# Optimization experiments

Measured on AMD Instinct MI355X. Metric: run time of the kernel, lower is better.

## Reference

```python
import jax, jax.numpy as jnp
import numpy as np

B, N, D = 2, 2048, 1024   # batch, seq, input_dim
H, DK, DV = 8, 128, 1024  # heads, qk_dim, v_dim (v_dim == input_dim for residual)


def setup_inputs() -> dict:
    key = jax.random.key(0)
    kx, kq, kk, kv = jax.random.split(key, 4)
    scale = 0.02
    x = jax.random.normal(kx, (B, N, D), dtype=jnp.float32)
    # torch nn.Linear weights are [out_features, in_features]; stacked over heads.
    Wq = jax.random.normal(kq, (H, DK, D), dtype=jnp.float32) * scale
    Wk = jax.random.normal(kk, (H, DK, D), dtype=jnp.float32) * scale
    Wv = jax.random.normal(kv, (H, DV, D), dtype=jnp.float32) * scale
    return {"x": x, "Wq": Wq, "Wk": Wk, "Wv": Wv}


def reference(x, Wq, Wk, Wv):
    # x: [B, N, D]; Wq/Wk: [H, DK, D]; Wv: [H, DV, D]
    n = x.shape[-2]
    Q = jnp.einsum('bnd,hed->bhne', x, Wq)  # [B,H,N,DK]
    K = jnp.einsum('bnd,hed->bhne', x, Wk)  # [B,H,N,DK]
    V = jnp.einsum('bnd,hvd->bhnv', x, Wv)  # [B,H,N,DV]
    scores = jnp.einsum('bhne,bhme->bhnm', Q, K)  # [B,H,N,N]
    # causal mask: masked entries set to mask_value=0.0, then relu, then /N
    causal = jnp.tril(jnp.ones((n, n), dtype=bool))
    sim = jnp.where(causal, jax.nn.relu(scores), jnp.float32(0.0)) / jnp.float32(n)
    # sum of per-head outputs added to residual
    head_out = jnp.einsum('bhnm,bhmv->bnv', sim, V)  # [B,N,DV]
    return x + head_out
```

## Files before the change

### kernel.cpp

```cpp
#include <hip/hip_runtime.h>

typedef __attribute__((ext_vector_type(8))) short bf16x8;
typedef __attribute__((ext_vector_type(4))) float floatx4;

__device__ __forceinline__ unsigned short f2bf(float f) {
  unsigned int u = __builtin_bit_cast(unsigned int, f);
  unsigned int r = (u + 0x7fffu + ((u >> 16) & 1u)) >> 16;
  return (unsigned short)r;
}

__device__ __forceinline__ unsigned int pack2(float a, float b) {
  return (unsigned int)f2bf(a) | ((unsigned int)f2bf(b) << 16);
}

__device__ __forceinline__ void gload16(const void* g, void* l) {
  __builtin_amdgcn_global_load_lds(
      (__attribute__((address_space(1))) void*)g,
      (__attribute__((address_space(3))) void*)l, 16, 0, 0);
}

__device__ __forceinline__ void barrier_v0_lgkm() {
  asm volatile("s_waitcnt vmcnt(0) lgkmcnt(0)" ::: "memory");
  __builtin_amdgcn_s_barrier();
  __builtin_amdgcn_sched_barrier(0);
}

__global__ __launch_bounds__(256) void convert_all(
    const float4* __restrict__ x4,
    const float4* __restrict__ wq4, const float4* __restrict__ wk4,
    const float4* __restrict__ wv4,
    uint2* __restrict__ xb4, uint2* __restrict__ wqkb4, uint2* __restrict__ wvb4,
    float4* __restrict__ out4)
{
  const int NX = 2 * 2048 * 1024 / 4;
  const int NQK = 8 * 256 * 1024 / 4;
  const int NV = 8 * 1024 * 1024 / 4;
  const int total = NX + NQK + NV;
  const float inv_n = 1.0f / 2048.0f;
  for (int i = blockIdx.x * 256 + threadIdx.x; i < total; i += gridDim.x * 256) {
    float4 f; uint2* dst;
    if (i < NX) {
      f = x4[i]; dst = &xb4[i];
      out4[i] = f;
    } else if (i < NX + NQK) {
      int j = i - NX;
      int c = j & 255;
      int row = j >> 8;
      int h = row >> 8, r = row & 255;
      f = (r < 128) ? wq4[(h * 128 + r) * 256 + c] : wk4[(h * 128 + r - 128) * 256 + c];
      dst = &wqkb4[j];
    } else {
      int j = i - NX - NQK;
      f = wv4[j];
      f.x *= inv_n; f.y *= inv_n; f.z *= inv_n; f.w *= inv_n;
      dst = &wvb4[j];
    }
    uint2 p; p.x = pack2(f.x, f.y); p.y = pack2(f.z, f.w);
    *dst = p;
  }
}

__global__ __launch_bounds__(256) void init_out(const float4* __restrict__ x,
                                                float4* __restrict__ out, int n4) {
  for (int i = blockIdx.x * 256 + threadIdx.x; i < n4; i += gridDim.x * 256)
    out[i] = x[i];
}

__device__ __forceinline__ void gemm_body(
    const unsigned short* __restrict__ Ag,
    const unsigned short* __restrict__ Bg,
    unsigned short* __restrict__ C, long ld,
    unsigned short* LA, unsigned short* LB, int t)
{
  const int l = t & 63, w = t >> 6;
  const int wr = w >> 1, wc = w & 1;
  const int l16 = l & 15, lq = l >> 4;
  floatx4 acc[4][4] = {};
  for (int k0 = 0; k0 < 1024; k0 += 64) {
    __syncthreads();
    for (int i = 0; i < 4; i++) {
      int cbase = i * 256 + (t & 192);
      int chunk = cbase + (t & 63);
      int row = chunk >> 3, c8 = chunk & 7;
      gload16(Ag + (long)row * 1024 + k0 + c8 * 8, &LA[cbase * 8]);
      gload16(Bg + (long)row * 1024 + k0 + c8 * 8, &LB[cbase * 8]);
    }
    __syncthreads();
    for (int kk = 0; kk < 2; kk++) {
      bf16x8 af[4], bfr[4];
      for (int m = 0; m < 4; m++)
        af[m]  = *reinterpret_cast<const bf16x8*>(&LA[(wr * 64 + m * 16 + l16) * 64 + kk * 32 + lq * 8]);
      for (int n = 0; n < 4; n++)
        bfr[n] = *reinterpret_cast<const bf16x8*>(&LB[(wc * 64 + n * 16 + l16) * 64 + kk * 32 + lq * 8]);
      for (int m = 0; m < 4; m++)
        for (int n = 0; n < 4; n++)
          acc[m][n] = __builtin_amdgcn_mfma_f32_16x16x32_bf16(af[m], bfr[n], acc[m][n], 0, 0, 0);
    }
  }
  for (int m = 0; m < 4; m++)
    for (int n = 0; n < 4; n++)
      for (int j = 0; j < 4; j++) {
        int row = wr * 64 + m * 16 + lq * 4 + j;
        int col = wc * 64 + n * 16 + l16;
        C[(long)row * ld + col] = f2bf(acc[m][n][j]);
      }
}

__global__ __launch_bounds__(256) void gemm_all(
    const unsigned short* __restrict__ xb,
    const unsigned short* __restrict__ Wqkb,
    const unsigned short* __restrict__ Wvb,
    unsigned short* __restrict__ Qb, unsigned short* __restrict__ Kb,
    unsigned short* __restrict__ Vtb)
{
  __shared__ __align__(16) unsigned short LA[128 * 64];
  __shared__ __align__(16) unsigned short LB[128 * 64];
  const int bid = blockIdx.x;
  const int t = threadIdx.x;
  if (bid < 512) {
    int bx = bid & 15, qy = (bid >> 4) & 1, z = bid >> 5;
    int b = z >> 3, h = z & 7;
    const unsigned short* Ag = xb + (long)b * 2048 * 1024 + (long)bx * 128 * 1024;
    const unsigned short* Bg = Wqkb + (long)h * 256 * 1024 + (long)qy * 128 * 1024;
    unsigned short* C = (qy ? Kb : Qb) + (long)z * 2048 * 128 + (long)bx * 128 * 128;
    gemm_body(Ag, Bg, C, 128, LA, LB, t);
  } else {
    int v = bid - 512;
    int by = v & 15, bx = (v >> 4) & 7, z = v >> 7;
    int b = z >> 3, h = z & 7;
    const unsigned short* Ag = Wvb + (long)h * 1024 * 1024 + (long)bx * 128 * 1024;
    const unsigned short* Bg = xb + (long)b * 2048 * 1024 + (long)by * 128 * 1024;
    unsigned short* C = Vtb + (long)z * 1024 * 2048 + (long)bx * 128 * 2048 + by * 128;
    gemm_body(Ag, Bg, C, 2048, LA, LB, t);
  }
}

__global__ __launch_bounds__(256) void gemm_bt(
    const float* __restrict__ Abase, long sAb, long sAh,
    const float* __restrict__ Bbase, long sBb, long sBh,
    unsigned short* __restrict__ Cbase, long sC,
    int M, int Nc, int K, int H, float cscale)
{
  int z = blockIdx.z;
  int b = z / H, h = z % H;
  const float* A  = Abase + (long)b * sAb + (long)h * sAh;
  const float* Bm = Bbase + (long)b * sBb + (long)h * sBh;
  unsigned short* C = Cbase + (long)z * sC;
  int tRow = blockIdx.x * 128;
  int tCol = blockIdx.y * 128;
  __shared__ __align__(16) unsigned short LA[128 * 72];
  __shared__ __align__(16) unsigned short LB[128 * 72];
  int t = threadIdx.x;
  int l = t & 63, w = t >> 6;
  int wr = w >> 1, wc = w & 1;
  int l16 = l & 15, lq = l >> 4;
  floatx4 acc[4][4] = {};
  for (int k0 = 0; k0 < K; k0 += 64) {
    __syncthreads();
    for (int i = 0; i < 8; i++) {
      int lin = i * 256 + t;
      int row = lin >> 4;
      int c4  = lin & 15;
      float4 va = *reinterpret_cast<const float4*>(A + (long)(tRow + row) * K + k0 + c4 * 4);
      uint2 pa; pa.x = pack2(va.x, va.y); pa.y = pack2(va.z, va.w);
      *reinterpret_cast<uint2*>(&LA[row * 72 + c4 * 4]) = pa;
      float4 vb = *reinterpret_cast<const float4*>(Bm + (long)(tCol + row) * K + k0 + c4 * 4);
      uint2 pb; pb.x = pack2(vb.x, vb.y); pb.y = pack2(vb.z, vb.w);
      *reinterpret_cast<uint2*>(&LB[row * 72 + c4 * 4]) = pb;
    }
    __syncthreads();
    for (int kk = 0; kk < 2; kk++) {
      bf16x8 af[4], bfr[4];
      for (int m = 0; m < 4; m++)
        af[m]  = *reinterpret_cast<const bf16x8*>(&LA[(wr * 64 + m * 16 + l16) * 72 + kk * 32 + lq * 8]);
      for (int n = 0; n < 4; n++)
        bfr[n] = *reinterpret_cast<const bf16x8*>(&LB[(wc * 64 + n * 16 + l16) * 72 + kk * 32 + lq * 8]);
      for (int m = 0; m < 4; m++)
        for (int n = 0; n < 4; n++)
          acc[m][n] = __builtin_amdgcn_mfma_f32_16x16x32_bf16(af[m], bfr[n], acc[m][n], 0, 0, 0);
    }
  }
  for (int m = 0; m < 4; m++)
    for (int n = 0; n < 4; n++)
      for (int j = 0; j < 4; j++) {
        int row = tRow + wr * 64 + m * 16 + lq * 4 + j;
        int col = tCol + wc * 64 + n * 16 + l16;
        C[(long)row * Nc + col] = f2bf(acc[m][n][j] * cscale);
      }
}

__global__ __launch_bounds__(256) void gemm_qk(
    const float* __restrict__ x,
    const float* __restrict__ Wq, const float* __restrict__ Wk,
    unsigned short* __restrict__ Qb, unsigned short* __restrict__ Kb)
{
  int z = blockIdx.z;
  int b = z >> 3, h = z & 7;
  const float* A  = x + (long)b * 2048 * 1024;
  const float* Bm = (blockIdx.y ? Wk : Wq) + (long)h * 128 * 1024;
  unsigned short* C = (blockIdx.y ? Kb : Qb) + (long)z * 2048 * 128;
  int tRow = blockIdx.x * 128;
  __shared__ __align__(16) unsigned short LA[128 * 72];
  __shared__ __align__(16) unsigned short LB[128 * 72];
  int t = threadIdx.x;
  int l = t & 63, w = t >> 6;
  int wr = w >> 1, wc = w & 1;
  int l16 = l & 15, lq = l >> 4;
  floatx4 acc[4][4] = {};
  const int K = 1024;
  for (int k0 = 0; k0 < K; k0 += 64) {
    __syncthreads();
    for (int i = 0; i < 8; i++) {
      int lin = i * 256 + t;
      int row = lin >> 4;
      int c4  = lin & 15;
      float4 va = *reinterpret_cast<const float4*>(A + (long)(tRow + row) * K + k0 + c4 * 4);
      uint2 pa; pa.x = pack2(va.x, va.y); pa.y = pack2(va.z, va.w);
      *reinterpret_cast<uint2*>(&LA[row * 72 + c4 * 4]) = pa;
      float4 vb = *reinterpret_cast<const float4*>(Bm + (long)row * K + k0 + c4 * 4);
      uint2 pb; pb.x = pack2(vb.x, vb.y); pb.y = pack2(vb.z, vb.w);
      *reinterpret_cast<uint2*>(&LB[row * 72 + c4 * 4]) = pb;
    }
    __syncthreads();
    for (int kk = 0; kk < 2; kk++) {
      bf16x8 af[4], bfr[4];
      for (int m = 0; m < 4; m++)
        af[m]  = *reinterpret_cast<const bf16x8*>(&LA[(wr * 64 + m * 16 + l16) * 72 + kk * 32 + lq * 8]);
      for (int n = 0; n < 4; n++)
        bfr[n] = *reinterpret_cast<const bf16x8*>(&LB[(wc * 64 + n * 16 + l16) * 72 + kk * 32 + lq * 8]);
      for (int m = 0; m < 4; m++)
        for (int n = 0; n < 4; n++)
          acc[m][n] = __builtin_amdgcn_mfma_f32_16x16x32_bf16(af[m], bfr[n], acc[m][n], 0, 0, 0);
    }
  }
  for (int m = 0; m < 4; m++)
    for (int n = 0; n < 4; n++)
      for (int j = 0; j < 4; j++) {
        int row = tRow + wr * 64 + m * 16 + lq * 4 + j;
        int col = wc * 64 + n * 16 + l16;
        C[(long)row * 128 + col] = f2bf(acc[m][n][j]);
      }
}

__global__ __launch_bounds__(256, 2) void attn_fused(
    const unsigned short* __restrict__ Qb,
    const unsigned short* __restrict__ Kb,
    const unsigned short* __restrict__ Vtb,
    float* __restrict__ out)
{
  const int bid = blockIdx.x;
  const int z = bid & 15;
  const int pair = (bid >> 4) & 15;
  const int vb = bid >> 8;
  const int b = z >> 3;
  const int t = threadIdx.x;
  const int l = t & 63, w = t >> 6;
  const int l16 = l & 15, lq = l >> 4;
  const int wm = w & 1, wn = w >> 1;
  const int swz = l16 & 7;

  __shared__ __align__(16) unsigned short LK[2][64 * 128];
  __shared__ __align__(16) unsigned short LV[256 * 64];
  __shared__ __align__(16) unsigned short LP[64 * 64];

  const unsigned short* Qz = Qb + (long)z * 2048 * 128;
  const unsigned short* Kh = Kb + (long)z * 2048 * 128;
  const unsigned short* Vh = Vtb + (long)z * 1024 * 2048 + (long)(vb * 256) * 2048;

  int ksrc[4], kdst[4];
#pragma unroll
  for (int i = 0; i < 4; i++) {
    int chunk = i * 256 + w * 64 + l;
    int r = chunk >> 4, c = chunk & 15;
    int cs = ((c & 7) ^ (r & 7)) | (c & 8);
    ksrc[i] = r * 128 + cs * 8;
    kdst[i] = (i * 256 + w * 64) * 8;
  }
  int vsrc[8], vdst[8];
#pragma unroll
  for (int i = 0; i < 8; i++) {
    int chunk = i * 256 + w * 64 + l;
    int r = chunk >> 3, c = chunk & 7;
    int cs = c ^ (r & 7);
    vsrc[i] = r * 2048 + cs * 8;
    vdst[i] = (i * 256 + w * 64) * 8;
  }

  int cur = 0;
  for (int hf = 0; hf < 2; hf++) {
    const int T = hf ? (31 - pair) : pair;
    const unsigned short* Qh = Qz + (long)T * 64 * 128;
    bf16x8 aQ[2][4];
#pragma unroll
    for (int sn = 0; sn < 2; sn++)
#pragma unroll
      for (int ke = 0; ke < 4; ke++)
        aQ[sn][ke] = *reinterpret_cast<const bf16x8*>(
            Qh + (long)(wn * 32 + sn * 16 + l16) * 128 + ke * 32 + lq * 8);
    floatx4 acc[4][4] = {};
#pragma unroll
    for (int i = 0; i < 4; i++)
      gload16(Kh + ksrc[i], &LK[cur][kdst[i]]);
    for (int M = 0; M <= T; M++) {
      barrier_v0_lgkm();
#pragma unroll
      for (int i = 0; i < 8; i++)
        gload16(Vh + M * 64 + vsrc[i], &LV[vdst[i]]);
      if (M < T) {
#pragma unroll
        for (int i = 0; i < 4; i++)
          gload16(Kh + (M + 1) * 8192 + ksrc[i], &LK[cur ^ 1][kdst[i]]);
      }
      const unsigned short* LKc = LK[cur];
      floatx4 sacc[2][2] = {{{}, {}}, {{}, {}}};
      __builtin_amdgcn_s_setprio(1);
#pragma unroll
      for (int ke = 0; ke < 4; ke++) {
        bf16x8 kf[2];
#pragma unroll
        for (int sm = 0; sm < 2; sm++) {
          int chunk = 4 * ke + lq;
          kf[sm] = *reinterpret_cast<const bf16x8*>(
              &LKc[(wm * 32 + sm * 16 + l16) * 128 +
                   ((((chunk & 7) ^ swz) | (chunk & 8)) * 8)]);
        }
#pragma unroll
        for (int sm = 0; sm < 2; sm++)
#pragma unroll
          for (int sn = 0; sn < 2; sn++)
            sacc[sm][sn] = __builtin_amdgcn_mfma_f32_16x16x32_bf16(
                kf[sm], aQ[sn][ke], sacc[sm][sn], 0, 0, 0);
      }
      __builtin_amdgcn_s_setprio(0);
      const bool diag = (M == T);
#pragma unroll
      for (int sm = 0; sm < 2; sm++)
#pragma unroll
        for (int sn = 0; sn < 2; sn++) {
          floatx4 v = sacc[sm][sn];
          float f0 = fmaxf(v[0], 0.0f), f1 = fmaxf(v[1], 0.0f);
          float f2 = fmaxf(v[2], 0.0f), f3 = fmaxf(v[3], 0.0f);
          if (diag) {
            int mm = wm * 32 + sm * 16 + lq * 4;
            int nn = wn * 32 + sn * 16 + l16;
            if (mm + 0 > nn) f0 = 0.0f;
            if (mm + 1 > nn) f1 = 0.0f;
            if (mm + 2 > nn) f2 = 0.0f;
            if (mm + 3 > nn) f3 = 0.0f;
          }
          unsigned int p0, p1;
          asm("v_cvt_pk_bf16_f32 %0, %1, %2" : "=v"(p0) : "v"(f0), "v"(f1));
          asm("v_cvt_pk_bf16_f32 %0, %1, %2" : "=v"(p1) : "v"(f2), "v"(f3));
          uint2 pk; pk.x = p0; pk.y = p1;
          int row = wn * 32 + sn * 16 + l16;
          int cs = wm * 32 + sm * 16 + lq * 4;
          *reinterpret_cast<uint2*>(
              &LP[row * 64 + (((cs >> 3) ^ (row & 7)) * 8) + (cs & 7)]) = pk;
        }
      if (M < T) {
        asm volatile("s_waitcnt vmcnt(4) lgkmcnt(0)" ::: "memory");
      } else {
        asm volatile("s_waitcnt vmcnt(0) lgkmcnt(0)" ::: "memory");
      }
      __builtin_amdgcn_s_barrier();
      __builtin_amdgcn_sched_barrier(0);
      __builtin_amdgcn_s_setprio(1);
#pragma unroll
      for (int km = 0; km < 2; km++) {
        bf16x8 aP[4], bV[4];
#pragma unroll
        for (int nf = 0; nf < 4; nf++)
          aP[nf] = *reinterpret_cast<const bf16x8*>(
              &LP[(nf * 16 + l16) * 64 + (((4 * km + lq) ^ swz) * 8)]);
#pragma unroll
        for (int vf = 0; vf < 4; vf++)
          bV[vf] = *reinterpret_cast<const bf16x8*>(
              &LV[(w * 64 + vf * 16 + l16) * 64 + (((4 * km + lq) ^ swz) * 8)]);
#pragma unroll
        for (int nf = 0; nf < 4; nf++)
#pragma unroll
          for (int vf = 0; vf < 4; vf++)
            acc[nf][vf] = __builtin_amdgcn_mfma_f32_16x16x32_bf16(
                aP[nf], bV[vf], acc[nf][vf], 0, 0, 0);
      }
      __builtin_amdgcn_s_setprio(0);
      cur ^= 1;
    }
#pragma unroll
    for (int nf = 0; nf < 4; nf++)
#pragma unroll
      for (int vf = 0; vf < 4; vf++)
#pragma unroll
        for (int j = 0; j < 4; j++) {
          int n = T * 64 + nf * 16 + lq * 4 + j;
          int v = vb * 256 + w * 64 + vf * 16 + l16;
          long idx = ((long)b * 2048 + n) * 1024 + v;
          unsafeAtomicAdd(&out[idx], acc[nf][vf][j]);
        }
  }
}

extern "C" void kernel_launch(void* const* d_in, const int* in_sizes, int n_in,
                              void* d_out, int out_size, void* d_ws, size_t ws_size,
                              hipStream_t stream) {
  const float* x  = (const float*)d_in[0];
  const float* Wq = (const float*)d_in[1];
  const float* Wk = (const float*)d_in[2];
  const float* Wv = (const float*)d_in[3];
  float* out = (float*)d_out;
  const size_t MB = 1u << 20;
  dim3 blk(256);

  if (ws_size >= 104 * MB) {
    unsigned short* Vtb  = (unsigned short*)d_ws;
    unsigned short* Wqkb = (unsigned short*)d_ws;
    unsigned short* Qb   = (unsigned short*)((char*)d_ws + 64 * MB);
    unsigned short* Kb   = (unsigned short*)((char*)d_ws + 72 * MB);
    unsigned short* xb   = (unsigned short*)((char*)d_ws + 80 * MB);
    unsigned short* Wvb  = (unsigned short*)((char*)d_ws + 88 * MB);

    convert_all<<<dim3(2048), blk, 0, stream>>>(
        (const float4*)x, (const float4*)Wq, (const float4*)Wk, (const float4*)Wv,
        (uint2*)xb, (uint2*)Wqkb, (uint2*)Wvb, (float4*)out);
    gemm_all<<<dim3(2560), blk, 0, stream>>>(xb, Wqkb, Wvb, Qb, Kb, Vtb);
    attn_fused<<<dim3(1024), blk, 0, stream>>>(Qb, Kb, Vtb, out);
  } else {
    unsigned short* Qb  = (unsigned short*)d_ws;
    unsigned short* Kb  = Qb + (size_t)2 * 8 * 2048 * 128;
    unsigned short* Vtb = Kb + (size_t)2 * 8 * 2048 * 128;
    init_out<<<dim3(1024), blk, 0, stream>>>(
        (const float4*)x, (float4*)out, 2 * 2048 * 1024 / 4);
    gemm_qk<<<dim3(16, 2, 16), blk, 0, stream>>>(x, Wq, Wk, Qb, Kb);
    gemm_bt<<<dim3(8, 16, 16), blk, 0, stream>>>(
        Wv, 0, (long)1024 * 1024, x, (long)2048 * 1024, 0,
        Vtb, (long)1024 * 2048, 1024, 2048, 1024, 8, 1.0f / 2048.0f);
    attn_fused<<<dim3(1024), blk, 0, stream>>>(Qb, Kb, Vtb, out);
  }
}
```

Before: 298.9 us.

## Replace projection GEMM with 256x256-tile, 8-wave, double-buffered pipelined kernel

```diff
diff --git a/kernel.cpp b/kernel.cpp
--- a/kernel.cpp
+++ b/kernel.cpp
@@ -66,73 +66,170 @@
     out[i] = x[i];
 }
 
-__device__ __forceinline__ void gemm_body(
-    const unsigned short* __restrict__ Ag,
-    const unsigned short* __restrict__ Bg,
-    unsigned short* __restrict__ C, long ld,
-    unsigned short* LA, unsigned short* LB, int t)
-{
-  const int l = t & 63, w = t >> 6;
-  const int wr = w >> 1, wc = w & 1;
-  const int l16 = l & 15, lq = l >> 4;
-  floatx4 acc[4][4] = {};
-  for (int k0 = 0; k0 < 1024; k0 += 64) {
-    __syncthreads();
-    for (int i = 0; i < 4; i++) {
-      int cbase = i * 256 + (t & 192);
-      int chunk = cbase + (t & 63);
-      int row = chunk >> 3, c8 = chunk & 7;
-      gload16(Ag + (long)row * 1024 + k0 + c8 * 8, &LA[cbase * 8]);
-      gload16(Bg + (long)row * 1024 + k0 + c8 * 8, &LB[cbase * 8]);
-    }
-    __syncthreads();
-    for (int kk = 0; kk < 2; kk++) {
-      bf16x8 af[4], bfr[4];
-      for (int m = 0; m < 4; m++)
-        af[m]  = *reinterpret_cast<const bf16x8*>(&LA[(wr * 64 + m * 16 + l16) * 64 + kk * 32 + lq * 8]);
-      for (int n = 0; n < 4; n++)
-        bfr[n] = *reinterpret_cast<const bf16x8*>(&LB[(wc * 64 + n * 16 + l16) * 64 + kk * 32 + lq * 8]);
-      for (int m = 0; m < 4; m++)
-        for (int n = 0; n < 4; n++)
-          acc[m][n] = __builtin_amdgcn_mfma_f32_16x16x32_bf16(af[m], bfr[n], acc[m][n], 0, 0, 0);
-    }
-  }
-  for (int m = 0; m < 4; m++)
-    for (int n = 0; n < 4; n++)
-      for (int j = 0; j < 4; j++) {
-        int row = wr * 64 + m * 16 + lq * 4 + j;
-        int col = wc * 64 + n * 16 + l16;
-        C[(long)row * ld + col] = f2bf(acc[m][n][j]);
-      }
-}
-
-__global__ __launch_bounds__(256) void gemm_all(
+__global__ __launch_bounds__(512, 2) void gemm8(
     const unsigned short* __restrict__ xb,
     const unsigned short* __restrict__ Wqkb,
     const unsigned short* __restrict__ Wvb,
     unsigned short* __restrict__ Qb, unsigned short* __restrict__ Kb,
     unsigned short* __restrict__ Vtb)
 {
-  __shared__ __align__(16) unsigned short LA[128 * 64];
-  __shared__ __align__(16) unsigned short LB[128 * 64];
+  __shared__ __align__(16) unsigned short LA[2][2][128 * 64];
+  __shared__ __align__(16) unsigned short LB[2][2][128 * 64];
   const int bid = blockIdx.x;
   const int t = threadIdx.x;
-  if (bid < 512) {
-    int bx = bid & 15, qy = (bid >> 4) & 1, z = bid >> 5;
+  const int l = t & 63, w = t >> 6;
+  const int l16 = l & 15, lq = l >> 4;
+  const int wm = w & 1, wn = w >> 1;
+
+  const unsigned short *Ag, *Bg;
+  unsigned short *C0, *C1; long ld0, ld1; int split;
+  if (bid < 128) {
+    int z = bid & 15, br = bid >> 4;
     int b = z >> 3, h = z & 7;
-    const unsigned short* Ag = xb + (long)b * 2048 * 1024 + (long)bx * 128 * 1024;
-    const unsigned short* Bg = Wqkb + (long)h * 256 * 1024 + (long)qy * 128 * 1024;
-    unsigned short* C = (qy ? Kb : Qb) + (long)z * 2048 * 128 + (long)bx * 128 * 128;
-    gemm_body(Ag, Bg, C, 128, LA, LB, t);
+    Ag = xb + (long)b * 2048 * 1024 + (long)br * 256 * 1024;
+    Bg = Wqkb + (long)h * 256 * 1024;
+    C0 = Qb + (long)z * 2048 * 128 + (long)br * 256 * 128;
+    C1 = Kb + (long)z * 2048 * 128 + (long)br * 256 * 128;
+    ld0 = 128; ld1 = 128; split = 128;
   } else {
-    int v = bid - 512;
-    int by = v & 15, bx = (v >> 4) & 7, z = v >> 7;
+    int v = bid - 128;
+    int z = v & 15, rc = v >> 4;
+    int bx = rc & 3, by = rc >> 2;
     int b = z >> 3, h = z & 7;
-    const unsigned short* Ag = Wvb + (long)h * 1024 * 1024 + (long)bx * 128 * 1024;
-    const unsigned short* Bg = xb + (long)b * 2048 * 1024 + (long)by * 128 * 1024;
-    unsigned short* C = Vtb + (long)z * 1024 * 2048 + (long)bx * 128 * 2048 + by * 128;
-    gemm_body(Ag, Bg, C, 2048, LA, LB, t);
-  }
+    Ag = Wvb + (long)h * 1024 * 1024 + (long)bx * 256 * 1024;
+    Bg = xb + (long)b * 2048 * 1024 + (long)by * 256 * 1024;
+    C0 = Vtb + (long)z * 1024 * 2048 + (long)bx * 256 * 2048 + by * 256;
+    C1 = C0; ld0 = 2048; ld1 = 2048; split = 1 << 30;
+  }
+
+  int rr[2], kk[2], cb[2];
+#pragma unroll
+  for (int i = 0; i < 2; i++) {
+    int c = i * 512 + t;
+    rr[i] = c >> 3;
+    int k8 = c & 7;
+    kk[i] = (k8 ^ (((rr[i] >> 2) & 3) << 1)) * 8;
+    cb[i] = (i * 512 + w * 64) * 8;
+  }
+  auto STAGE = [&](const unsigned short* OP, unsigned short* dstbuf, int kt, int half) {
+#pragma unroll
+    for (int i = 0; i < 2; i++)
+      gload16(OP + (long)(half * 128 + rr[i]) * 1024 + kt * 64 + kk[i],
+              dstbuf + cb[i]);
+  };
+  auto RD = [&](const unsigned short* buf, int fr, int ks) -> bf16x8 {
+    int r = fr * 16 + l16;
+    int k8 = ks * 4 + lq;
+    int k8s = k8 ^ (((r >> 2) & 3) << 1);
+    return *reinterpret_cast<const bf16x8*>(buf + r * 64 + k8s * 8);
+  };
+
+  floatx4 acc[8][4] = {};
+  const int bfr = (wn & 1) * 4;
+
+  STAGE(Ag, LA[0][0], 0, 0); STAGE(Ag, LA[0][1], 0, 1);
+  STAGE(Bg, LB[0][0], 0, 0); STAGE(Bg, LB[0][1], 0, 1);
+  asm volatile("s_waitcnt vmcnt(0)" ::: "memory");
+  __builtin_amdgcn_s_barrier();
+  __builtin_amdgcn_sched_barrier(0);
+
+  for (int kt = 0; kt < 16; kt++) {
+    const int d = kt & 1, nd = d ^ 1;
+    const unsigned short* myA = LA[d][wm];
+    const unsigned short* myB = LB[d][wn >> 1];
+    const bool more = (kt + 1 < 16);
+    bf16x8 a0[4][2], a1[4][2], b0[2][2], b1[2][2];
+
+#pragma unroll
+    for (int fr = 0; fr < 4; fr++)
+#pragma unroll
+      for (int ks = 0; ks < 2; ks++) a0[fr][ks] = RD(myA, fr, ks);
+#pragma unroll
+    for (int fc = 0; fc < 2; fc++)
+#pragma unroll
+      for (int ks = 0; ks < 2; ks++) b0[fc][ks] = RD(myB, bfr + fc, ks);
+    if (more) { STAGE(Ag, LA[nd][0], kt + 1, 0); STAGE(Ag, LA[nd][1], kt + 1, 1); }
+    __builtin_amdgcn_s_barrier();
+    asm volatile("s_waitcnt lgkmcnt(0)" ::: "memory");
+    __builtin_amdgcn_sched_barrier(0);
+    __builtin_amdgcn_s_setprio(1);
+#pragma unroll
+    for (int fr = 0; fr < 4; fr++)
+#pragma unroll
+      for (int fc = 0; fc < 2; fc++)
+#pragma unroll
+        for (int ks = 0; ks < 2; ks++)
+          acc[fr][fc] = __builtin_amdgcn_mfma_f32_16x16x32_bf16(
+              a0[fr][ks], b0[fc][ks], acc[fr][fc], 0, 0, 0);
+    __builtin_amdgcn_s_setprio(0);
+    __builtin_amdgcn_s_barrier();
+
+#pragma unroll
+    for (int fc = 0; fc < 2; fc++)
+#pragma unroll
+      for (int ks = 0; ks < 2; ks++) b1[fc][ks] = RD(myB, bfr + 2 + fc, ks);
+    if (more) { STAGE(Bg, LB[nd][0], kt + 1, 0); STAGE(Bg, LB[nd][1], kt + 1, 1); }
+    __builtin_amdgcn_s_barrier();
+    asm volatile("s_waitcnt lgkmcnt(0)" ::: "memory");
+    __builtin_amdgcn_sched_barrier(0);
+    __builtin_amdgcn_s_setprio(1);
+#pragma unroll
+    for (int fr = 0; fr < 4; fr++)
+#pragma unroll
+      for (int fc = 0; fc < 2; fc++)
+#pragma unroll
+        for (int ks = 0; ks < 2; ks++)
+          acc[fr][2 + fc] = __builtin_amdgcn_mfma_f32_16x16x32_bf16(
+              a0[fr][ks], b1[fc][ks], acc[fr][2 + fc], 0, 0, 0);
+    __builtin_amdgcn_s_setprio(0);
+    __builtin_amdgcn_s_barrier();
+
+#pragma unroll
+    for (int fr = 0; fr < 4; fr++)
+#pragma unroll
+      for (int ks = 0; ks < 2; ks++) a1[fr][ks] = RD(myA, 4 + fr, ks);
+    __builtin_amdgcn_s_barrier();
+    asm volatile("s_waitcnt lgkmcnt(0)" ::: "memory");
+    __builtin_amdgcn_sched_barrier(0);
+    __builtin_amdgcn_s_setprio(1);
+#pragma unroll
+    for (int fr = 0; fr < 4; fr++)
+#pragma unroll
+      for (int fc = 0; fc < 2; fc++)
+#pragma unroll
+        for (int ks = 0; ks < 2; ks++)
+          acc[4 + fr][fc] = __builtin_amdgcn_mfma_f32_16x16x32_bf16(
+              a1[fr][ks], b0[fc][ks], acc[4 + fr][fc], 0, 0, 0);
+    __builtin_amdgcn_s_setprio(0);
+    __builtin_amdgcn_s_barrier();
+
+    __builtin_amdgcn_s_setprio(1);
+#pragma unroll
+    for (int fr = 0; fr < 4; fr++)
+#pragma unroll
+      for (int fc = 0; fc < 2; fc++)
+#pragma unroll
+        for (int ks = 0; ks < 2; ks++)
+          acc[4 + fr][2 + fc] = __builtin_amdgcn_mfma_f32_16x16x32_bf16(
+              a1[fr][ks], b1[fc][ks], acc[4 + fr][2 + fc], 0, 0, 0);
+    __builtin_amdgcn_s_setprio(0);
+    asm volatile("s_waitcnt vmcnt(0)" ::: "memory");
+    __builtin_amdgcn_s_barrier();
+    __builtin_amdgcn_sched_barrier(0);
+  }
+
+#pragma unroll
+  for (int fr = 0; fr < 8; fr++)
+#pragma unroll
+    for (int fc = 0; fc < 4; fc++)
+#pragma unroll
+      for (int j = 0; j < 4; j++) {
+        int row = wm * 128 + fr * 16 + lq * 4 + j;
+        int col = wn * 64 + fc * 16 + l16;
+        unsigned short v = f2bf(acc[fr][fc][j]);
+        if (col < split) C0[(long)row * ld0 + col] = v;
+        else             C1[(long)row * ld1 + (col - split)] = v;
+      }
 }
 
 __global__ __launch_bounds__(256) void gemm_bt(
@@ -422,7 +519,7 @@
     convert_all<<<dim3(2048), blk, 0, stream>>>(
         (const float4*)x, (const float4*)Wq, (const float4*)Wk, (const float4*)Wv,
         (uint2*)xb, (uint2*)Wqkb, (uint2*)Wvb, (float4*)out);
-    gemm_all<<<dim3(2560), blk, 0, stream>>>(xb, Wqkb, Wvb, Qb, Kb, Vtb);
+    gemm8<<<dim3(640), dim3(512), 0, stream>>>(xb, Wqkb, Wvb, Qb, Kb, Vtb);
     attn_fused<<<dim3(1024), blk, 0, stream>>>(Qb, Kb, Vtb, out);
   } else {
     unsigned short* Qb  = (unsigned short*)d_ws;
```

Measured after the change: 277.5 us (median of 5 runs). -7.2%, faster.
